# Kernel tuning notes

Hardware: AMD Instinct MI355X
Metric: run time of the kernel (lower is better)

Reference implementation:

```python
import jax, jax.numpy as jnp
import numpy as np

I, O, R = 64, 64, 896          # input / output / regulatory protein counts
N = I + O + R                  # total GRN size
WARMUP = 25                    # warmup_count


def setup_inputs() -> dict:
    key = jax.random.key(0)
    k1, k2, k3, k4 = jax.random.split(key, 4)
    return {
        "inputs": jax.random.uniform(k1, (16384, I), dtype=jnp.float32),
        "identifiers": jax.random.uniform(k2, (N,), dtype=jnp.float32),
        "enhancers": jax.random.uniform(k3, (N,), dtype=jnp.float32),
        "inhibitors": jax.random.uniform(k4, (N,), dtype=jnp.float32),
        "beta": jnp.full((1,), 2.0, dtype=jnp.float32),
        "delta": jnp.full((1,), 1.0, dtype=jnp.float32),
    }


def _signatures(identifiers, enhancers, inhibitors, beta):
    # sig[j, i] = exp(-beta * |tag_j - id_i|): affinity of protein j regulating protein i.
    enh = jnp.exp(-beta * jnp.abs(enhancers[:, None] - identifiers[None, :]))
    inh = jnp.exp(-beta * jnp.abs(inhibitors[:, None] - identifiers[None, :]))
    # output proteins do not regulate others -> zero their rows
    mask = jnp.ones((N,), dtype=enh.dtype).at[I:I + O].set(0.0)[:, None]
    return enh * mask, inh * mask


def _step(conc, sig_diff, delta):
    # conc: [..., N]; sig_diff = enh_sigs - inh_sigs: [N, N]
    dc = (delta / N) * (conc @ sig_diff)
    new = jnp.maximum(conc + dc, 0.0)
    reg = new[..., I:]                                    # outputs + regulatory
    s = jnp.sum(reg, axis=-1, keepdims=True)
    reg = jnp.where(s > 0, reg / s, reg)                  # renormalize
    return jnp.concatenate([conc[..., :I], reg], axis=-1)  # inputs clamped


def reference(inputs, identifiers, enhancers, inhibitors, beta, delta):
    b, d = beta[0], delta[0]
    enh_s, inh_s = _signatures(identifiers, enhancers, inhibitors, b)
    sig_diff = enh_s - inh_s

    # setup(): uniform initial concentrations; warmup(): shared sequential steps
    conc0 = jnp.full((N,), 1.0 / N, dtype=jnp.float32)
    def warm(c, _):
        return _step(c, sig_diff, d), None
    conc, _ = jax.lax.scan(warm, conc0, None, length=WARMUP)

    # per-sample (batched instead of tf.map_fn): set input concs, one step
    B = inputs.shape[0]
    batch_conc = jnp.concatenate(
        [inputs, jnp.broadcast_to(conc[I:], (B, N - I))], axis=-1)
    new = _step(batch_conc, sig_diff, d)
    return new[..., I:I + O]  # output protein concentrations [B, O]
```

## Files before the change

### kernel.cpp

```cpp
#include <hip/hip_runtime.h>
#include <math.h>

#define NJ 960
#define NSRC 896
#define NWARM 25

typedef unsigned long long u64;
typedef unsigned int u32;

#define RK_O   0u
#define CT_O   896u
#define HD_O   1856u
#define WK_F   8192u
#define BASE_F (WK_F + 64u * 960u)

#define TAG_RK 0x524B0001u
#define TAG_CT 0x43540001u
#define TAG_HD 0x48440001u

__device__ __forceinline__ void ast(u64* p, u64 v) {
  __hip_atomic_store(p, v, __ATOMIC_RELAXED, __HIP_MEMORY_SCOPE_AGENT);
}
__device__ __forceinline__ u64 ald(const u64* p) {
  return __hip_atomic_load(p, __ATOMIC_RELAXED, __HIP_MEMORY_SCOPE_AGENT);
}
__device__ __forceinline__ u32 poll32(const u64* p, u32 tag) {
  u64 v = ald(p);
  while ((u32)(v >> 32) != tag) { __builtin_amdgcn_s_sleep(1); v = ald(p); }
  return (u32)v;
}

__global__ __launch_bounds__(256) void front_k(const float* __restrict__ ident,
                                               const float* __restrict__ enh,
                                               const float* __restrict__ inh,
                                               const float* __restrict__ beta,
                                               const float* __restrict__ delta,
                                               void* __restrict__ wsv) {
  u64* RK = (u64*)wsv + RK_O;
  u64* CT = (u64*)wsv + CT_O;
  u64* HD = (u64*)wsv + HD_O;
  float* Wk = (float*)wsv + WK_F;
  float* base = (float*)wsv + BASE_F;

  const int tid = threadIdx.x;
  const float bb = beta[0];
  const float dN = delta[0] / 1024.0f;

  if (blockIdx.x > 0) {
    const int g = (blockIdx.x - 1) * 256 + tid;
    const int c8 = g & 7;
    if (g < NSRC * 8) {
      int m = g >> 3;
      float myE = enh[128 + m], myI = inh[128 + m];
      int re = 0, ri = 0;
      for (int i = 112 * c8; i < 112 * c8 + 112; ++i) {
        float ev = enh[128 + i], iv = inh[128 + i];
        re += (ev < myE || (ev == myE && i < m)) ? 1 : 0;
        ri += (iv < myI || (iv == myI && i < m)) ? 1 : 0;
      }
      int p = re | (ri << 16);
      p += __shfl_xor(p, 1); p += __shfl_xor(p, 2); p += __shfl_xor(p, 4);
      if (c8 == 0) ast(&RK[m], ((u64)TAG_RK << 32) | (u32)p);
    }
    {
      int j = g >> 3;
      float cj = ident[64 + j];
      int ce = 0, ci = 0;
      for (int i = 112 * c8; i < 112 * c8 + 112; ++i) {
        ce += (enh[128 + i] <= cj) ? 1 : 0;
        ci += (inh[128 + i] <= cj) ? 1 : 0;
      }
      int p = ce | (ci << 16);
      p += __shfl_xor(p, 1); p += __shfl_xor(p, 2); p += __shfl_xor(p, 4);
      if (c8 == 0) ast(&CT[j], ((u64)TAG_CT << 32) | (u32)p);
    }
    {
      int j = g >> 3;
      float cj = ident[64 + j];
      float h = 0.0f;
      for (int k = 8 * c8; k < 8 * c8 + 8; ++k)
        h += expf(-bb * fabsf(enh[k] - cj)) - expf(-bb * fabsf(inh[k] - cj));
      h += __shfl_xor(h, 1); h += __shfl_xor(h, 2); h += __shfl_xor(h, 4);
      if (c8 == 0)
        ast(&HD[j], ((u64)TAG_HD << 32) |
                    (u64)__float_as_uint(dN * h * (1.0f / 1024.0f)));
    }
    {
      int k = g / 120;
      int jb = (g % 120) * 8;
      float ek = enh[k], ik = inh[k];
      #pragma unroll
      for (int u = 0; u < 8; ++u) {
        float cj = ident[64 + jb + u];
        Wk[(size_t)k * NJ + jb + u] =
            dN * (expf(-bb * fabsf(ek - cj)) - expf(-bb * fabsf(ik - cj)));
      }
    }
    return;
  }

  __shared__ float yl[NJ];
  __shared__ float2 scanE[1024];
  __shared__ float2 scanI[1024];
  __shared__ float4 wtot[4];
  __shared__ float ssw[4];

  const int lane = tid & 63, wvid = tid >> 6;

  int rE[4], rI[4];
  if (tid < 224) {
    #pragma unroll
    for (int s = 0; s < 4; ++s) {
      u32 v = poll32(&RK[4 * tid + s], TAG_RK);
      rE[s] = v & 0xFFFF; rI[s] = v >> 16;
    }
  }
  int cE[4], cI[4];
  float hd[4], fm[4], fp[4];
  if (tid < 240) {
    #pragma unroll
    for (int c = 0; c < 4; ++c) {
      u32 v = poll32(&CT[4 * tid + c], TAG_CT);
      cE[c] = v & 0xFFFF; cI[c] = v >> 16;
      hd[c] = __uint_as_float(poll32(&HD[4 * tid + c], TAG_HD));
      float cj = ident[64 + 4 * tid + c];
      fm[c] = expf(-bb * cj); fp[c] = expf(bb * cj);
    }
  }
  float EP[4], EN[4], IP[4], IN2[4];
  if (tid < 224) {
    #pragma unroll
    for (int s = 0; s < 4; ++s) {
      float e = enh[128 + 4 * tid + s], i2 = inh[128 + 4 * tid + s];
      EP[s] = expf(bb * e);  EN[s] = expf(-bb * e);
      IP[s] = expf(bb * i2); IN2[s] = expf(-bb * i2);
    }
  }
  float y_own[4] = {1.0f / 1024.0f, 1.0f / 1024.0f, 1.0f / 1024.0f, 1.0f / 1024.0f};
  if (tid < 240) {
    #pragma unroll
    for (int c = 0; c < 4; ++c) yl[4 * tid + c] = 1.0f / 1024.0f;
  }
  __syncthreads();

  for (int t = 0; t <= NWARM; ++t) {
    if (tid == 0) {
      scanE[0] = make_float2(0.f, 0.f);
      scanI[0] = make_float2(0.f, 0.f);
    }
    if (tid >= 224) {
      #pragma unroll
      for (int c = 0; c < 4; ++c) {
        int p = 4 * tid + c;
        if (p > NSRC) {
          scanE[p] = make_float2(0.f, 0.f);
          scanI[p] = make_float2(0.f, 0.f);
        }
      }
    }
    if (tid < 224) {
      #pragma unroll
      for (int s = 0; s < 4; ++s) {
        float ym = yl[64 + 4 * tid + s];
        scanE[rE[s] + 1] = make_float2(ym * EP[s], ym * EN[s]);
        scanI[rI[s] + 1] = make_float2(ym * IP[s], ym * IN2[s]);
      }
    }
    __syncthreads();

    float2 e0 = scanE[4 * tid], e1 = scanE[4 * tid + 1],
           e2 = scanE[4 * tid + 2], e3 = scanE[4 * tid + 3];
    float2 i0 = scanI[4 * tid], i1 = scanI[4 * tid + 1],
           i2v = scanI[4 * tid + 2], i3 = scanI[4 * tid + 3];
    e1.x += e0.x; e1.y += e0.y; e2.x += e1.x; e2.y += e1.y; e3.x += e2.x; e3.y += e2.y;
    i1.x += i0.x; i1.y += i0.y; i2v.x += i1.x; i2v.y += i1.y; i3.x += i2v.x; i3.y += i2v.y;
    float4 tot = make_float4(e3.x, e3.y, i3.x, i3.y);
    float4 inc = tot;
    #pragma unroll
    for (int off = 1; off < 64; off <<= 1) {
      float ox = __shfl_up(inc.x, off, 64);
      float oy = __shfl_up(inc.y, off, 64);
      float oz = __shfl_up(inc.z, off, 64);
      float ow = __shfl_up(inc.w, off, 64);
      if (lane >= off) { inc.x += ox; inc.y += oy; inc.z += oz; inc.w += ow; }
    }
    if (lane == 63) wtot[wvid] = inc;
    __syncthreads();
    float4 exc = make_float4(inc.x - tot.x, inc.y - tot.y,
                             inc.z - tot.z, inc.w - tot.w);
    #pragma unroll
    for (int w = 0; w < 3; ++w)
      if (w < wvid) {
        float4 p = wtot[w];
        exc.x += p.x; exc.y += p.y; exc.z += p.z; exc.w += p.w;
      }
    e0.x += exc.x; e0.y += exc.y; e1.x += exc.x; e1.y += exc.y;
    e2.x += exc.x; e2.y += exc.y; e3.x += exc.x; e3.y += exc.y;
    i0.x += exc.z; i0.y += exc.w; i1.x += exc.z; i1.y += exc.w;
    i2v.x += exc.z; i2v.y += exc.w; i3.x += exc.z; i3.y += exc.w;
    scanE[4 * tid] = e0; scanE[4 * tid + 1] = e1;
    scanE[4 * tid + 2] = e2; scanE[4 * tid + 3] = e3;
    scanI[4 * tid] = i0; scanI[4 * tid + 1] = i1;
    scanI[4 * tid + 2] = i2v; scanI[4 * tid + 3] = i3;
    __syncthreads();

    float nv[4] = {0.f, 0.f, 0.f, 0.f};
    float psum = 0.0f;
    if (tid < 240) {
      float2 TE = scanE[NSRC], TI = scanI[NSRC];
      #pragma unroll
      for (int c = 0; c < 4; ++c) {
        float2 AE = scanE[cE[c]], AI = scanI[cI[c]];
        float dot = fm[c] * AE.x + fp[c] * (TE.y - AE.y)
                  - fm[c] * AI.x - fp[c] * (TI.y - AI.y);
        float pre = y_own[c] + dN * dot;
        if (t < NWARM) {
          nv[c] = fmaxf(pre + hd[c], 0.0f);
          psum += nv[c];
        } else {
          base[4 * tid + c] = pre;
        }
      }
    }
    if (t < NWARM) {
      #pragma unroll
      for (int off = 32; off >= 1; off >>= 1) psum += __shfl_xor(psum, off);
      if (lane == 0) ssw[wvid] = psum;
      __syncthreads();
      float s = ssw[0] + ssw[1] + ssw[2] + ssw[3];
      float inv = (s > 0.0f) ? 1.0f / s : 1.0f;
      if (tid < 240) {
        #pragma unroll
        for (int c = 0; c < 4; ++c) {
          y_own[c] = nv[c] * inv;
          yl[4 * tid + c] = y_own[c];
        }
      }
    }
    __syncthreads();
  }
}

__global__ __launch_bounds__(512) void batch_t(const float* __restrict__ inp,
                                               const float* __restrict__ ws,
                                               float* __restrict__ out) {
  __shared__ float At[64][66];
  __shared__ float Wl[16][516];
  __shared__ float bch[512];

  const int tid = threadIdx.x;
  const int colg = tid & 63;
  const int rowg = tid >> 6;
  const size_t rowbase = (size_t)blockIdx.x * 64;
  const float* __restrict__ Wk = ws + WK_F;
  const float* __restrict__ base = ws + BASE_F;

  #pragma unroll
  for (int i = 0; i < 2; ++i) {
    int fi = tid + i * 512;
    int r = fi >> 4, c4 = (fi & 15) * 4;
    float4 f4 = *(const float4*)(inp + (rowbase + r) * 64 + c4);
    At[c4 + 0][r] = f4.x; At[c4 + 1][r] = f4.y;
    At[c4 + 2][r] = f4.z; At[c4 + 3][r] = f4.w;
  }

  float rs[8];
  #pragma unroll
  for (int r = 0; r < 8; ++r) rs[r] = 0.0f;
  float acc[8][8];

  #pragma unroll 1
  for (int ch = 0; ch < 2; ++ch) {
    const int c0 = ch ? 0 : 512;
    #pragma unroll
    for (int r = 0; r < 8; ++r)
      #pragma unroll
      for (int c = 0; c < 8; ++c) acc[r][c] = 0.0f;

    __syncthreads();
    {
      int j = c0 + tid;
      bch[tid] = (j < 960) ? base[j] : -1.0e30f;
    }

    #pragma unroll 1
    for (int s = 0; s < 4; ++s) {
      __syncthreads();
      #pragma unroll
      for (int i = 0; i < 4; ++i) {
        int fi = tid + i * 512;
        int kk = fi >> 7;
        int c4 = (fi & 127) * 4;
        int j = c0 + c4;
        float4 v = make_float4(0.f, 0.f, 0.f, 0.f);
        if (j < 960)
          v = *(const float4*)(Wk + (size_t)(16 * s + kk) * NJ + j);
        *(float4*)&Wl[kk][c4] = v;
      }
      __syncthreads();

      #pragma unroll
      for (int kk = 0; kk < 16; ++kk) {
        float4 a0 = *(const float4*)&At[16 * s + kk][rowg * 8];
        float4 a1 = *(const float4*)&At[16 * s + kk][rowg * 8 + 4];
        float4 w0 = *(const float4*)&Wl[kk][colg * 8];
        float4 w1 = *(const float4*)&Wl[kk][colg * 8 + 4];
        float a[8] = {a0.x, a0.y, a0.z, a0.w, a1.x, a1.y, a1.z, a1.w};
        float w[8] = {w0.x, w0.y, w0.z, w0.w, w1.x, w1.y, w1.z, w1.w};
        #pragma unroll
        for (int r = 0; r < 8; ++r)
          #pragma unroll
          for (int c = 0; c < 8; ++c)
            acc[r][c] = fmaf(a[r], w[c], acc[r][c]);
      }
    }

    #pragma unroll
    for (int c = 0; c < 8; ++c) {
      float bv = bch[colg * 8 + c];
      #pragma unroll
      for (int r = 0; r < 8; ++r)
        rs[r] += fmaxf(acc[r][c] + bv, 0.0f);
    }
  }

  #pragma unroll
  for (int r = 0; r < 8; ++r) {
    float v = rs[r];
    #pragma unroll
    for (int off = 32; off >= 1; off >>= 1) v += __shfl_xor(v, off);
    rs[r] = v;
  }

  if (colg < 8) {
    #pragma unroll
    for (int r = 0; r < 8; ++r) {
      float inv = (rs[r] > 0.0f) ? 1.0f / rs[r] : 1.0f;
      float* op = out + (rowbase + rowg * 8 + r) * 64 + colg * 8;
      float4 o;
      o.x = fmaxf(acc[r][0] + bch[colg * 8 + 0], 0.0f) * inv;
      o.y = fmaxf(acc[r][1] + bch[colg * 8 + 1], 0.0f) * inv;
      o.z = fmaxf(acc[r][2] + bch[colg * 8 + 2], 0.0f) * inv;
      o.w = fmaxf(acc[r][3] + bch[colg * 8 + 3], 0.0f) * inv;
      *(float4*)op = o;
      o.x = fmaxf(acc[r][4] + bch[colg * 8 + 4], 0.0f) * inv;
      o.y = fmaxf(acc[r][5] + bch[colg * 8 + 5], 0.0f) * inv;
      o.z = fmaxf(acc[r][6] + bch[colg * 8 + 6], 0.0f) * inv;
      o.w = fmaxf(acc[r][7] + bch[colg * 8 + 7], 0.0f) * inv;
      *(float4*)(op + 4) = o;
    }
  }
}

extern "C" void kernel_launch(void* const* d_in, const int* in_sizes, int n_in,
                              void* d_out, int out_size, void* d_ws, size_t ws_size,
                              hipStream_t stream) {
  const float* inp   = (const float*)d_in[0];
  const float* ident = (const float*)d_in[1];
  const float* enh   = (const float*)d_in[2];
  const float* inh   = (const float*)d_in[3];
  const float* beta  = (const float*)d_in[4];
  const float* delta = (const float*)d_in[5];

  hipLaunchKernelGGL(front_k, dim3(31), dim3(256), 0, stream,
                     ident, enh, inh, beta, delta, d_ws);
  hipLaunchKernelGGL(batch_t, dim3(256), dim3(512), 0, stream,
                     inp, (const float*)d_ws, (float*)d_out);
}
```

Baseline: 158.8 us.

## Fuse warmup and batch kernels into one launch with flag-based handoff

Merges the front (rank/count/warmup) kernel and the batch GEMM kernel into a single launch. One block runs the 25-step warmup scan in a single wavefront at raised priority, using wave-level fences instead of block barriers. Batch blocks compute their weight tiles on the fly from enh/inh/ident rather than reading a precomputed Wk matrix, and poll tagged flags for the warmup-produced bias only after their GEMM finishes, so the GEMM overlaps the serial warmup. The spin-wait handoff assumes the warmup block is resident alongside the batch blocks, and the batch blocks now repeat exp work that was previously done once.

Result: slower. 275.6 us (+73.5%).

```diff
diff --git a/kernel.cpp b/kernel.cpp
--- a/kernel.cpp
+++ b/kernel.cpp
@@ -4,19 +4,23 @@
 #define NJ 960
 #define NSRC 896
 #define NWARM 25
+#define NPREP 15
+#define NBATCH 256
 
 typedef unsigned long long u64;
 typedef unsigned int u32;
 
-#define RK_O   0u
-#define CT_O   896u
-#define HD_O   1856u
-#define WK_F   8192u
-#define BASE_F (WK_F + 64u * 960u)
+#define RK_O 0u
+#define CT_O 896u
+#define HD_O 1856u
+#define BS_O 2816u
 
 #define TAG_RK 0x524B0001u
 #define TAG_CT 0x43540001u
 #define TAG_HD 0x48440001u
+#define TAG_BS 0x42530001u
+
+#define WAVE_FENCE __asm__ __volatile__("s_waitcnt lgkmcnt(0)" ::: "memory")
 
 __device__ __forceinline__ void ast(u64* p, u64 v) {
   __hip_atomic_store(p, v, __ATOMIC_RELAXED, __HIP_MEMORY_SCOPE_AGENT);
@@ -30,24 +34,155 @@
   return (u32)v;
 }
 
-__global__ __launch_bounds__(256) void front_k(const float* __restrict__ ident,
-                                               const float* __restrict__ enh,
-                                               const float* __restrict__ inh,
-                                               const float* __restrict__ beta,
-                                               const float* __restrict__ delta,
-                                               void* __restrict__ wsv) {
+struct BatchS {
+  float At[64][66];
+  float Wl[16][516];
+  float bch[512];
+  float cid[512];
+  float he[64], hi[64];
+};
+struct FrontS {
+  float4 TR[896];
+  float2 scE[960];
+  float2 scI[960];
+  float4 colc[960];
+  float yl[960];
+};
+
+__global__ __launch_bounds__(512, 4) void fused_k(
+    const float* __restrict__ inp, const float* __restrict__ ident,
+    const float* __restrict__ enh, const float* __restrict__ inh,
+    const float* __restrict__ beta, const float* __restrict__ delta,
+    void* __restrict__ wsv, float* __restrict__ out) {
+  __shared__ __align__(16) char smraw[sizeof(BatchS)];
+
   u64* RK = (u64*)wsv + RK_O;
   u64* CT = (u64*)wsv + CT_O;
   u64* HD = (u64*)wsv + HD_O;
-  float* Wk = (float*)wsv + WK_F;
-  float* base = (float*)wsv + BASE_F;
+  u64* BS = (u64*)wsv + BS_O;
 
   const int tid = threadIdx.x;
+  const int bid = blockIdx.x;
   const float bb = beta[0];
   const float dN = delta[0] / 1024.0f;
 
-  if (blockIdx.x > 0) {
-    const int g = (blockIdx.x - 1) * 256 + tid;
+  if (bid == 0) {
+    if (tid >= 64) return;
+    __asm__ __volatile__("s_setprio 3");
+    FrontS& F = *(FrontS*)smraw;
+    const int lane = tid;
+
+    u32 rEI[14];
+    #pragma unroll
+    for (int s = 0; s < 14; ++s) {
+      int m = lane * 14 + s;
+      rEI[s] = poll32(&RK[m], TAG_RK);
+      float e = enh[128 + m], iv = inh[128 + m];
+      F.TR[m] = make_float4(expf(bb * e), expf(-bb * e),
+                            expf(bb * iv), expf(-bb * iv));
+    }
+    float y[15];
+    #pragma unroll
+    for (int c = 0; c < 15; ++c) {
+      int j = lane * 15 + c;
+      u32 ct = poll32(&CT[j], TAG_CT);
+      float hdv = __uint_as_float(poll32(&HD[j], TAG_HD));
+      float cj = ident[64 + j];
+      F.colc[j] = make_float4(expf(-bb * cj), expf(bb * cj), hdv,
+                              __uint_as_float(ct));
+      y[c] = 1.0f / 1024.0f;
+      F.yl[j] = 1.0f / 1024.0f;
+    }
+    WAVE_FENCE;
+
+    for (int t = 0; t <= NWARM; ++t) {
+      if (lane < 63) {
+        F.scE[897 + lane] = make_float2(0.f, 0.f);
+        F.scI[897 + lane] = make_float2(0.f, 0.f);
+      } else {
+        F.scE[0] = make_float2(0.f, 0.f);
+        F.scI[0] = make_float2(0.f, 0.f);
+      }
+      float ym[14];
+      #pragma unroll
+      for (int s = 0; s < 14; ++s) ym[s] = F.yl[64 + lane * 14 + s];
+      #pragma unroll
+      for (int s = 0; s < 14; ++s) {
+        float4 tr = F.TR[lane * 14 + s];
+        u32 r = rEI[s];
+        F.scE[(r & 0xFFFF) + 1] = make_float2(ym[s] * tr.x, ym[s] * tr.y);
+        F.scI[(r >> 16) + 1]    = make_float2(ym[s] * tr.z, ym[s] * tr.w);
+      }
+      WAVE_FENCE;
+
+      const int p0 = lane * 15;
+      float2 pe[15], pi[15];
+      #pragma unroll
+      for (int i = 0; i < 15; ++i) { pe[i] = F.scE[p0 + i]; pi[i] = F.scI[p0 + i]; }
+      #pragma unroll
+      for (int i = 1; i < 15; ++i) {
+        pe[i].x += pe[i - 1].x; pe[i].y += pe[i - 1].y;
+        pi[i].x += pi[i - 1].x; pi[i].y += pi[i - 1].y;
+      }
+      float4 tot = make_float4(pe[14].x, pe[14].y, pi[14].x, pi[14].y);
+      float4 inc = tot;
+      #pragma unroll
+      for (int off = 1; off < 64; off <<= 1) {
+        float ox = __shfl_up(inc.x, off, 64);
+        float oy = __shfl_up(inc.y, off, 64);
+        float oz = __shfl_up(inc.z, off, 64);
+        float ow = __shfl_up(inc.w, off, 64);
+        if (lane >= off) { inc.x += ox; inc.y += oy; inc.z += oz; inc.w += ow; }
+      }
+      float4 exc = make_float4(inc.x - tot.x, inc.y - tot.y,
+                               inc.z - tot.z, inc.w - tot.w);
+      #pragma unroll
+      for (int i = 0; i < 15; ++i) {
+        pe[i].x += exc.x; pe[i].y += exc.y;
+        pi[i].x += exc.z; pi[i].y += exc.w;
+      }
+      float TEy = __shfl(inc.y, 63);
+      float TIy = __shfl(inc.w, 63);
+      #pragma unroll
+      for (int i = 0; i < 15; ++i) { F.scE[p0 + i] = pe[i]; F.scI[p0 + i] = pi[i]; }
+      WAVE_FENCE;
+
+      float nv[15];
+      float psum = 0.0f;
+      #pragma unroll
+      for (int c = 0; c < 15; ++c) {
+        int j = lane * 15 + c;
+        float4 cc = F.colc[j];
+        u32 ct = __float_as_uint(cc.w);
+        float2 AE = F.scE[ct & 0xFFFF];
+        float2 AI = F.scI[ct >> 16];
+        float dot = cc.x * AE.x + cc.y * (TEy - AE.y)
+                  - cc.x * AI.x - cc.y * (TIy - AI.y);
+        float pre = y[c] + dN * dot;
+        if (t < NWARM) {
+          nv[c] = fmaxf(pre + cc.z, 0.0f);
+          psum += nv[c];
+        } else {
+          ast(&BS[j], ((u64)TAG_BS << 32) | (u64)__float_as_uint(pre));
+        }
+      }
+      if (t < NWARM) {
+        #pragma unroll
+        for (int off = 32; off >= 1; off >>= 1) psum += __shfl_xor(psum, off);
+        float inv = (psum > 0.0f) ? 1.0f / psum : 1.0f;
+        #pragma unroll
+        for (int c = 0; c < 15; ++c) {
+          y[c] = nv[c] * inv;
+          F.yl[lane * 15 + c] = y[c];
+        }
+      }
+      WAVE_FENCE;
+    }
+    return;
+  }
+
+  if (bid <= NPREP) {
+    const int g = (bid - 1) * 512 + tid;
     const int c8 = g & 7;
     if (g < NSRC * 8) {
       int m = g >> 3;
@@ -85,183 +220,23 @@
         ast(&HD[j], ((u64)TAG_HD << 32) |
                     (u64)__float_as_uint(dN * h * (1.0f / 1024.0f)));
     }
-    {
-      int k = g / 120;
-      int jb = (g % 120) * 8;
-      float ek = enh[k], ik = inh[k];
-      #pragma unroll
-      for (int u = 0; u < 8; ++u) {
-        float cj = ident[64 + jb + u];
-        Wk[(size_t)k * NJ + jb + u] =
-            dN * (expf(-bb * fabsf(ek - cj)) - expf(-bb * fabsf(ik - cj)));
-      }
-    }
     return;
   }
 
-  __shared__ float yl[NJ];
-  __shared__ float2 scanE[1024];
-  __shared__ float2 scanI[1024];
-  __shared__ float4 wtot[4];
-  __shared__ float ssw[4];
-
-  const int lane = tid & 63, wvid = tid >> 6;
-
-  int rE[4], rI[4];
-  if (tid < 224) {
-    #pragma unroll
-    for (int s = 0; s < 4; ++s) {
-      u32 v = poll32(&RK[4 * tid + s], TAG_RK);
-      rE[s] = v & 0xFFFF; rI[s] = v >> 16;
-    }
-  }
-  int cE[4], cI[4];
-  float hd[4], fm[4], fp[4];
-  if (tid < 240) {
-    #pragma unroll
-    for (int c = 0; c < 4; ++c) {
-      u32 v = poll32(&CT[4 * tid + c], TAG_CT);
-      cE[c] = v & 0xFFFF; cI[c] = v >> 16;
-      hd[c] = __uint_as_float(poll32(&HD[4 * tid + c], TAG_HD));
-      float cj = ident[64 + 4 * tid + c];
-      fm[c] = expf(-bb * cj); fp[c] = expf(bb * cj);
-    }
-  }
-  float EP[4], EN[4], IP[4], IN2[4];
-  if (tid < 224) {
-    #pragma unroll
-    for (int s = 0; s < 4; ++s) {
-      float e = enh[128 + 4 * tid + s], i2 = inh[128 + 4 * tid + s];
-      EP[s] = expf(bb * e);  EN[s] = expf(-bb * e);
-      IP[s] = expf(bb * i2); IN2[s] = expf(-bb * i2);
-    }
-  }
-  float y_own[4] = {1.0f / 1024.0f, 1.0f / 1024.0f, 1.0f / 1024.0f, 1.0f / 1024.0f};
-  if (tid < 240) {
-    #pragma unroll
-    for (int c = 0; c < 4; ++c) yl[4 * tid + c] = 1.0f / 1024.0f;
-  }
-  __syncthreads();
-
-  for (int t = 0; t <= NWARM; ++t) {
-    if (tid == 0) {
-      scanE[0] = make_float2(0.f, 0.f);
-      scanI[0] = make_float2(0.f, 0.f);
-    }
-    if (tid >= 224) {
-      #pragma unroll
-      for (int c = 0; c < 4; ++c) {
-        int p = 4 * tid + c;
-        if (p > NSRC) {
-          scanE[p] = make_float2(0.f, 0.f);
-          scanI[p] = make_float2(0.f, 0.f);
-        }
-      }
-    }
-    if (tid < 224) {
-      #pragma unroll
-      for (int s = 0; s < 4; ++s) {
-        float ym = yl[64 + 4 * tid + s];
-        scanE[rE[s] + 1] = make_float2(ym * EP[s], ym * EN[s]);
-        scanI[rI[s] + 1] = make_float2(ym * IP[s], ym * IN2[s]);
-      }
-    }
-    __syncthreads();
-
-    float2 e0 = scanE[4 * tid], e1 = scanE[4 * tid + 1],
-           e2 = scanE[4 * tid + 2], e3 = scanE[4 * tid + 3];
-    float2 i0 = scanI[4 * tid], i1 = scanI[4 * tid + 1],
-           i2v = scanI[4 * tid + 2], i3 = scanI[4 * tid + 3];
-    e1.x += e0.x; e1.y += e0.y; e2.x += e1.x; e2.y += e1.y; e3.x += e2.x; e3.y += e2.y;
-    i1.x += i0.x; i1.y += i0.y; i2v.x += i1.x; i2v.y += i1.y; i3.x += i2v.x; i3.y += i2v.y;
-    float4 tot = make_float4(e3.x, e3.y, i3.x, i3.y);
-    float4 inc = tot;
-    #pragma unroll
-    for (int off = 1; off < 64; off <<= 1) {
-      float ox = __shfl_up(inc.x, off, 64);
-      float oy = __shfl_up(inc.y, off, 64);
-      float oz = __shfl_up(inc.z, off, 64);
-      float ow = __shfl_up(inc.w, off, 64);
-      if (lane >= off) { inc.x += ox; inc.y += oy; inc.z += oz; inc.w += ow; }
-    }
-    if (lane == 63) wtot[wvid] = inc;
-    __syncthreads();
-    float4 exc = make_float4(inc.x - tot.x, inc.y - tot.y,
-                             inc.z - tot.z, inc.w - tot.w);
-    #pragma unroll
-    for (int w = 0; w < 3; ++w)
-      if (w < wvid) {
-        float4 p = wtot[w];
-        exc.x += p.x; exc.y += p.y; exc.z += p.z; exc.w += p.w;
-      }
-    e0.x += exc.x; e0.y += exc.y; e1.x += exc.x; e1.y += exc.y;
-    e2.x += exc.x; e2.y += exc.y; e3.x += exc.x; e3.y += exc.y;
-    i0.x += exc.z; i0.y += exc.w; i1.x += exc.z; i1.y += exc.w;
-    i2v.x += exc.z; i2v.y += exc.w; i3.x += exc.z; i3.y += exc.w;
-    scanE[4 * tid] = e0; scanE[4 * tid + 1] = e1;
-    scanE[4 * tid + 2] = e2; scanE[4 * tid + 3] = e3;
-    scanI[4 * tid] = i0; scanI[4 * tid + 1] = i1;
-    scanI[4 * tid + 2] = i2v; scanI[4 * tid + 3] = i3;
-    __syncthreads();
-
-    float nv[4] = {0.f, 0.f, 0.f, 0.f};
-    float psum = 0.0f;
-    if (tid < 240) {
-      float2 TE = scanE[NSRC], TI = scanI[NSRC];
-      #pragma unroll
-      for (int c = 0; c < 4; ++c) {
-        float2 AE = scanE[cE[c]], AI = scanI[cI[c]];
-        float dot = fm[c] * AE.x + fp[c] * (TE.y - AE.y)
-                  - fm[c] * AI.x - fp[c] * (TI.y - AI.y);
-        float pre = y_own[c] + dN * dot;
-        if (t < NWARM) {
-          nv[c] = fmaxf(pre + hd[c], 0.0f);
-          psum += nv[c];
-        } else {
-          base[4 * tid + c] = pre;
-        }
-      }
-    }
-    if (t < NWARM) {
-      #pragma unroll
-      for (int off = 32; off >= 1; off >>= 1) psum += __shfl_xor(psum, off);
-      if (lane == 0) ssw[wvid] = psum;
-      __syncthreads();
-      float s = ssw[0] + ssw[1] + ssw[2] + ssw[3];
-      float inv = (s > 0.0f) ? 1.0f / s : 1.0f;
-      if (tid < 240) {
-        #pragma unroll
-        for (int c = 0; c < 4; ++c) {
-          y_own[c] = nv[c] * inv;
-          yl[4 * tid + c] = y_own[c];
-        }
-      }
-    }
-    __syncthreads();
-  }
-}
-
-__global__ __launch_bounds__(512) void batch_t(const float* __restrict__ inp,
-                                               const float* __restrict__ ws,
-                                               float* __restrict__ out) {
-  __shared__ float At[64][66];
-  __shared__ float Wl[16][516];
-  __shared__ float bch[512];
-
-  const int tid = threadIdx.x;
+  BatchS& S = *(BatchS*)smraw;
+  const int bx = bid - 1 - NPREP;
   const int colg = tid & 63;
   const int rowg = tid >> 6;
-  const size_t rowbase = (size_t)blockIdx.x * 64;
-  const float* __restrict__ Wk = ws + WK_F;
-  const float* __restrict__ base = ws + BASE_F;
-
+  const size_t rowbase = (size_t)bx * 64;
+
+  if (tid < 64) { S.he[tid] = enh[tid]; S.hi[tid] = inh[tid]; }
   #pragma unroll
   for (int i = 0; i < 2; ++i) {
     int fi = tid + i * 512;
     int r = fi >> 4, c4 = (fi & 15) * 4;
     float4 f4 = *(const float4*)(inp + (rowbase + r) * 64 + c4);
-    At[c4 + 0][r] = f4.x; At[c4 + 1][r] = f4.y;
-    At[c4 + 2][r] = f4.z; At[c4 + 3][r] = f4.w;
+    S.At[c4 + 0][r] = f4.x; S.At[c4 + 1][r] = f4.y;
+    S.At[c4 + 2][r] = f4.z; S.At[c4 + 3][r] = f4.w;
   }
 
   float rs[8];
@@ -272,39 +247,37 @@
   #pragma unroll 1
   for (int ch = 0; ch < 2; ++ch) {
     const int c0 = ch ? 0 : 512;
+    { int j = c0 + tid; S.cid[tid] = (j < 960) ? ident[64 + j] : 0.0f; }
     #pragma unroll
     for (int r = 0; r < 8; ++r)
       #pragma unroll
       for (int c = 0; c < 8; ++c) acc[r][c] = 0.0f;
-
-    __syncthreads();
-    {
-      int j = c0 + tid;
-      bch[tid] = (j < 960) ? base[j] : -1.0e30f;
-    }
 
     #pragma unroll 1
     for (int s = 0; s < 4; ++s) {
       __syncthreads();
-      #pragma unroll
-      for (int i = 0; i < 4; ++i) {
-        int fi = tid + i * 512;
-        int kk = fi >> 7;
-        int c4 = (fi & 127) * 4;
-        int j = c0 + c4;
-        float4 v = make_float4(0.f, 0.f, 0.f, 0.f);
-        if (j < 960)
-          v = *(const float4*)(Wk + (size_t)(16 * s + kk) * NJ + j);
-        *(float4*)&Wl[kk][c4] = v;
+      {
+        const int j = c0 + tid;
+        const float cj = S.cid[tid];
+        const bool ok = (j < 960);
+        #pragma unroll
+        for (int i2 = 0; i2 < 16; ++i2) {
+          int k = 16 * s + i2;
+          float v = 0.0f;
+          if (ok)
+            v = dN * (expf(-bb * fabsf(S.he[k] - cj)) -
+                      expf(-bb * fabsf(S.hi[k] - cj)));
+          S.Wl[i2][tid] = v;
+        }
       }
       __syncthreads();
 
       #pragma unroll
       for (int kk = 0; kk < 16; ++kk) {
-        float4 a0 = *(const float4*)&At[16 * s + kk][rowg * 8];
-        float4 a1 = *(const float4*)&At[16 * s + kk][rowg * 8 + 4];
-        float4 w0 = *(const float4*)&Wl[kk][colg * 8];
-        float4 w1 = *(const float4*)&Wl[kk][colg * 8 + 4];
+        float4 a0 = *(const float4*)&S.At[16 * s + kk][rowg * 8];
+        float4 a1 = *(const float4*)&S.At[16 * s + kk][rowg * 8 + 4];
+        float4 w0 = *(const float4*)&S.Wl[kk][colg * 8];
+        float4 w1 = *(const float4*)&S.Wl[kk][colg * 8 + 4];
         float a[8] = {a0.x, a0.y, a0.z, a0.w, a1.x, a1.y, a1.z, a1.w};
         float w[8] = {w0.x, w0.y, w0.z, w0.w, w1.x, w1.y, w1.z, w1.w};
         #pragma unroll
@@ -315,9 +288,14 @@
       }
     }
 
+    { int j = c0 + tid;
+      float bv = -1.0e30f;
+      if (j < 960) bv = __uint_as_float(poll32(&BS[j], TAG_BS));
+      S.bch[tid] = bv; }
+    __syncthreads();
     #pragma unroll
     for (int c = 0; c < 8; ++c) {
-      float bv = bch[colg * 8 + c];
+      float bv = S.bch[colg * 8 + c];
       #pragma unroll
       for (int r = 0; r < 8; ++r)
         rs[r] += fmaxf(acc[r][c] + bv, 0.0f);
@@ -338,15 +316,15 @@
       float inv = (rs[r] > 0.0f) ? 1.0f / rs[r] : 1.0f;
       float* op = out + (rowbase + rowg * 8 + r) * 64 + colg * 8;
       float4 o;
-      o.x = fmaxf(acc[r][0] + bch[colg * 8 + 0], 0.0f) * inv;
-      o.y = fmaxf(acc[r][1] + bch[colg * 8 + 1], 0.0f) * inv;
-      o.z = fmaxf(acc[r][2] + bch[colg * 8 + 2], 0.0f) * inv;
-      o.w = fmaxf(acc[r][3] + bch[colg * 8 + 3], 0.0f) * inv;
+      o.x = fmaxf(acc[r][0] + S.bch[colg * 8 + 0], 0.0f) * inv;
+      o.y = fmaxf(acc[r][1] + S.bch[colg * 8 + 1], 0.0f) * inv;
+      o.z = fmaxf(acc[r][2] + S.bch[colg * 8 + 2], 0.0f) * inv;
+      o.w = fmaxf(acc[r][3] + S.bch[colg * 8 + 3], 0.0f) * inv;
       *(float4*)op = o;
-      o.x = fmaxf(acc[r][4] + bch[colg * 8 + 4], 0.0f) * inv;
-      o.y = fmaxf(acc[r][5] + bch[colg * 8 + 5], 0.0f) * inv;
-      o.z = fmaxf(acc[r][6] + bch[colg * 8 + 6], 0.0f) * inv;
-      o.w = fmaxf(acc[r][7] + bch[colg * 8 + 7], 0.0f) * inv;
+      o.x = fmaxf(acc[r][4] + S.bch[colg * 8 + 4], 0.0f) * inv;
+      o.y = fmaxf(acc[r][5] + S.bch[colg * 8 + 5], 0.0f) * inv;
+      o.z = fmaxf(acc[r][6] + S.bch[colg * 8 + 6], 0.0f) * inv;
+      o.w = fmaxf(acc[r][7] + S.bch[colg * 8 + 7], 0.0f) * inv;
       *(float4*)(op + 4) = o;
     }
   }
@@ -362,8 +340,6 @@
   const float* beta  = (const float*)d_in[4];
   const float* delta = (const float*)d_in[5];
 
-  hipLaunchKernelGGL(front_k, dim3(31), dim3(256), 0, stream,
-                     ident, enh, inh, beta, delta, d_ws);
-  hipLaunchKernelGGL(batch_t, dim3(256), dim3(512), 0, stream,
-                     inp, (const float*)d_ws, (float*)d_out);
-}
+  hipLaunchKernelGGL(fused_k, dim3(1 + NPREP + NBATCH), dim3(512), 0, stream,
+                     inp, ident, enh, inh, beta, delta, d_ws, (float*)d_out);
+}
```
